# Performance work log

Measured on AMD Instinct MI355X. Metric: run time of the kernel, lower is better.

## Reference

```python
import jax, jax.numpy as jnp
import numpy as np

EPS = 1e-8  # torch.cosine_similarity norm clamp

def setup_inputs() -> dict:
    key = jax.random.key(0)
    k1, k2, k3, k4 = jax.random.split(key, 4)
    B, S, D, C = 64, 512, 768, 512
    V = jax.random.normal(k1, (B, S, D), dtype=jnp.float32)
    label_embeddings = jax.random.normal(k2, (C, D), dtype=jnp.float32)
    fc_w = jax.random.normal(k3, (C, D), dtype=jnp.float32) * 0.02
    fc_b = jax.random.normal(k4, (C,), dtype=jnp.float32) * 0.02
    return {"V": V, "label_embeddings": label_embeddings, "fc_w": fc_w, "fc_b": fc_b}

def reference(V, label_embeddings, fc_w, fc_b):
    # Normalized embeddings (cosine similarity = dot of unit vectors, norms clamped at EPS)
    Vn = V / jnp.maximum(jnp.linalg.norm(V, axis=-1, keepdims=True), EPS)
    Ln = label_embeddings / jnp.maximum(
        jnp.linalg.norm(label_embeddings, axis=-1, keepdims=True), EPS)
    # [B, S, C] cosine similarities, then max over classes -> per-token weight m [B, S]
    sims = jnp.einsum('bsd,cd->bsc', Vn, Ln)
    m = jnp.max(sims, axis=-1)
    # Softmax over sequence dim -> attention beta [B, S]
    beta = jax.nn.softmax(m, axis=-1)
    # Weighted sum of token embeddings: z = V^T beta  -> [B, D]
    z = jnp.einsum('bsd,bs->bd', V, beta)
    # Final classifier
    out = z @ fc_w.T + fc_b
    return (out, z)
```

## Files before the change

kernel.cpp:

```cpp
#include <hip/hip_runtime.h>
#include <cstdint>
#include <cstddef>

#define BB 64
#define SS 512
#define DD 768
#define CC 512

typedef __attribute__((ext_vector_type(8))) short short8;
typedef __attribute__((ext_vector_type(4))) float f32x4;

#define GLOBAL_AS __attribute__((address_space(1)))
#define LDS_AS __attribute__((address_space(3)))

static __device__ __forceinline__ unsigned short f2bf(float f) {
  union { float f; unsigned u; } v; v.f = f;
  unsigned u = v.u;
  u += 0x7FFFu + ((u >> 16) & 1u);
  return (unsigned short)(u >> 16);
}

static __device__ __forceinline__ void async_copy16(const void* g, void* l) {
  __builtin_amdgcn_global_load_lds((const GLOBAL_AS void*)g, (LDS_AS void*)l,
                                   16, 0, 0);
}

__global__ __launch_bounds__(256) void k_label_norm(const float* __restrict__ L,
                                                    unsigned short* __restrict__ Lnb) {
  const int c = blockIdx.x;
  const int tid = threadIdx.x;
  const float* row = L + (size_t)c * DD;
  float v[3];
  float s = 0.f;
#pragma unroll
  for (int k = 0; k < 3; k++) { v[k] = row[tid + 256 * k]; s += v[k] * v[k]; }
#pragma unroll
  for (int o = 32; o > 0; o >>= 1) s += __shfl_xor(s, o, 64);
  __shared__ float wsum[4];
  if ((tid & 63) == 0) wsum[tid >> 6] = s;
  __syncthreads();
  const float tot = wsum[0] + wsum[1] + wsum[2] + wsum[3];
  const float inv = 1.f / fmaxf(sqrtf(tot), 1e-8f);
  unsigned short* orow = Lnb + (size_t)c * DD;
  const int sw = c & 7;
#pragma unroll
  for (int k = 0; k < 3; k++) {
    const int d = tid + 256 * k;
    const int idx = (((d >> 3) ^ sw) << 3) | (d & 7);
    orow[idx] = f2bf(v[k] * inv);
  }
}

__global__ __launch_bounds__(512) void k_sims_max(const float* __restrict__ V,
                                                  const unsigned short* __restrict__ Lnb,
                                                  float* __restrict__ m_out) {
  const int tid = threadIdx.x;
  const int wave = tid >> 6;
  const int lane = tid & 63;
  const int q = lane >> 4;
  const int mr = lane & 15;
  const int64_t tokBase = (int64_t)blockIdx.x * 128 + wave * 16;

  __shared__ unsigned short Bs[2][16 * DD];
  __shared__ float nrmS[8][16];

  {
    const char* src = (const char*)Lnb;
    char* dst = (char*)&Bs[0][0];
#pragma unroll
    for (int i = wave; i < 24; i += 8)
      async_copy16(src + i * 1024 + lane * 16, dst + i * 1024);
  }

  const float* arow = V + (tokBase + mr) * DD + q * 8;
  short8 afrag[24];
  float nrm2 = 0.f;
#pragma unroll
  for (int kc = 0; kc < 24; kc++) {
    const float4* p = (const float4*)(arow + kc * 32);
    const float4 x = p[0];
    const float4 y = p[1];
    short8 a;
    a[0] = (short)f2bf(x.x); a[1] = (short)f2bf(x.y);
    a[2] = (short)f2bf(x.z); a[3] = (short)f2bf(x.w);
    a[4] = (short)f2bf(y.x); a[5] = (short)f2bf(y.y);
    a[6] = (short)f2bf(y.z); a[7] = (short)f2bf(y.w);
    afrag[kc] = a;
    nrm2 += x.x * x.x + x.y * x.y + x.z * x.z + x.w * x.w;
    nrm2 += y.x * y.x + y.y * y.y + y.z * y.z + y.w * y.w;
  }
  nrm2 += __shfl_xor(nrm2, 16, 64);
  nrm2 += __shfl_xor(nrm2, 32, 64);
  if (q == 0) nrmS[wave][mr] = nrm2;

  __syncthreads();

  const int swLo = mr & 3;
  const int swHi = (mr >> 2) & 1;
  const int elemBase = mr * DD + ((q ^ swLo) << 3);
  const int u0off = swHi ? 32 : 0;
  const int u1off = swHi ? 0 : 32;

  f32x4 vmax = {-3e38f, -3e38f, -3e38f, -3e38f};
  for (int cc = 0; cc < 32; cc++) {
    const int p = cc & 1;
    if (cc + 1 < 32) {
      const char* src = (const char*)(Lnb + (size_t)(cc + 1) * 16 * DD);
      char* dst = (char*)&Bs[p ^ 1][0];
#pragma unroll
      for (int i = wave; i < 24; i += 8)
        async_copy16(src + i * 1024 + lane * 16, dst + i * 1024);
    }
    const unsigned short* b0 = &Bs[p][elemBase + u0off];
    const unsigned short* b1 = &Bs[p][elemBase + u1off];
    f32x4 acc = {0.f, 0.f, 0.f, 0.f};
#pragma unroll
    for (int t = 0; t < 12; t++) {
      const short8 bu0 = *(const short8*)(b0 + t * 64);
      acc = __builtin_amdgcn_mfma_f32_16x16x32_bf16(afrag[2 * t], bu0, acc, 0, 0, 0);
      const short8 bu1 = *(const short8*)(b1 + t * 64);
      acc = __builtin_amdgcn_mfma_f32_16x16x32_bf16(afrag[2 * t + 1], bu1, acc, 0, 0, 0);
    }
    vmax[0] = fmaxf(vmax[0], acc[0]);
    vmax[1] = fmaxf(vmax[1], acc[1]);
    vmax[2] = fmaxf(vmax[2], acc[2]);
    vmax[3] = fmaxf(vmax[3], acc[3]);
    __syncthreads();
  }
#pragma unroll
  for (int o = 1; o < 16; o <<= 1) {
#pragma unroll
    for (int r = 0; r < 4; r++) vmax[r] = fmaxf(vmax[r], __shfl_xor(vmax[r], o, 64));
  }
  if (mr == 0) {
#pragma unroll
    for (int r = 0; r < 4; r++) {
      const float nr = nrmS[wave][q * 4 + r];
      m_out[tokBase + q * 4 + r] = vmax[r] / fmaxf(sqrtf(nr), 1e-8f);
    }
  }
}

__global__ __launch_bounds__(256) void k_softmax(const float* __restrict__ m,
                                                 float* __restrict__ beta) {
  const int b = blockIdx.x;
  const int tid = threadIdx.x;
  const float* mb = m + (size_t)b * SS;
  const float v0 = mb[tid];
  const float v1 = mb[tid + 256];
  float mx = fmaxf(v0, v1);
#pragma unroll
  for (int o = 32; o > 0; o >>= 1) mx = fmaxf(mx, __shfl_xor(mx, o, 64));
  __shared__ float wred[4];
  if ((tid & 63) == 0) wred[tid >> 6] = mx;
  __syncthreads();
  mx = fmaxf(fmaxf(wred[0], wred[1]), fmaxf(wred[2], wred[3]));
  const float e0 = __expf(v0 - mx);
  const float e1 = __expf(v1 - mx);
  float s = e0 + e1;
#pragma unroll
  for (int o = 32; o > 0; o >>= 1) s += __shfl_xor(s, o, 64);
  __syncthreads();
  if ((tid & 63) == 0) wred[tid >> 6] = s;
  __syncthreads();
  s = wred[0] + wred[1] + wred[2] + wred[3];
  const float inv = 1.f / s;
  float* bb = beta + (size_t)b * SS;
  bb[tid] = e0 * inv;
  bb[tid + 256] = e1 * inv;
}

__global__ __launch_bounds__(192) void k_zpart(const float* __restrict__ V,
                                               const float* __restrict__ beta,
                                               float* __restrict__ zpart,
                                               int spc, int nsc) {
  const int blk = blockIdx.x;
  const int b = blk / nsc;
  const int sc = blk % nsc;
  const int tid = threadIdx.x;
  const float* vb = V + ((size_t)b * SS + (size_t)sc * spc) * DD + tid * 4;
  const float* bb = beta + (size_t)b * SS + (size_t)sc * spc;
  float4 acc = {0.f, 0.f, 0.f, 0.f};
#pragma unroll 4
  for (int s = 0; s < spc; s++) {
    const float w = bb[s];
    const float4 x = *(const float4*)(vb + (size_t)s * DD);
    acc.x += w * x.x; acc.y += w * x.y; acc.z += w * x.z; acc.w += w * x.w;
  }
  *(float4*)(zpart + (size_t)blk * DD + tid * 4) = acc;
}

__global__ __launch_bounds__(256) void k_final(const float* __restrict__ zpart,
                                               const float* __restrict__ fc_w,
                                               const float* __restrict__ fc_b,
                                               float* __restrict__ out,
                                               float* __restrict__ zout,
                                               int nsc) {
  const int b = blockIdx.x >> 1;
  const int half = blockIdx.x & 1;
  const int tid = threadIdx.x;
  __shared__ float zs[DD];
  for (int i = tid; i < DD; i += 256) {
    float s = 0.f;
    for (int sc = 0; sc < nsc; sc++) s += zpart[((size_t)b * nsc + sc) * DD + i];
    zs[i] = s;
    if (half == 0) zout[(size_t)b * DD + i] = s;
  }
  __syncthreads();
  const int c = half * 256 + tid;
  const float4* w = (const float4*)(fc_w + (size_t)c * DD);
  float acc = 0.f;
  for (int d4 = 0; d4 < DD / 4; d4++) {
    const float4 ww = w[d4];
    acc += ww.x * zs[d4 * 4] + ww.y * zs[d4 * 4 + 1] +
           ww.z * zs[d4 * 4 + 2] + ww.w * zs[d4 * 4 + 3];
  }
  out[(size_t)b * CC + c] = acc + fc_b[c];
}

extern "C" void kernel_launch(void* const* d_in, const int* in_sizes, int n_in,
                              void* d_out, int out_size, void* d_ws, size_t ws_size,
                              hipStream_t stream) {
  const float* V  = (const float*)d_in[0];
  const float* L  = (const float*)d_in[1];
  const float* fw = (const float*)d_in[2];
  const float* fb = (const float*)d_in[3];
  float* out = (float*)d_out;

  char* ws = (char*)d_ws;
  unsigned short* Lnb = (unsigned short*)ws;
  float* m     = (float*)(ws + 786432);
  float* beta  = (float*)(ws + 917504);
  float* zpart = (float*)(ws + 1048576);

  const int nsc = (ws_size >= (size_t)1048576 + 16 * BB * DD * 4) ? 16 : 8;
  const int spc = SS / nsc;

  k_label_norm<<<CC, 256, 0, stream>>>(L, Lnb);
  k_sims_max<<<256, 512, 0, stream>>>(V, Lnb, m);
  k_softmax<<<BB, 256, 0, stream>>>(m, beta);
  k_zpart<<<BB * nsc, 192, 0, stream>>>(V, beta, zpart, spc, nsc);
  k_final<<<2 * BB, 256, 0, stream>>>(zpart, fw, fb, out, out + BB * CC, nsc);
}
```

Measured before the change: 247.4 us.

## Compute two 16-token tiles per wave in sims kernel, shrink blocks to 2 waves

Each wave in the cosine-sim max kernel now holds A fragments for 32 tokens (two 16-row tiles) and reuses each LDS-loaded label fragment for two MFMAs. Blocks shrink from 8 waves to 2 waves (64 tokens) and the grid doubles to 512 blocks. The aim is to cut LDS reads per MFMA and raise the number of independent accumulation chains. In exchange, register pressure roughly doubles (48 short8 fragments per lane), and each block now streams the whole label matrix for only 64 tokens. That doubles L2 traffic for Lnb and may lower occupancy.

```diff
diff --git a/kernel.cpp b/kernel.cpp
--- a/kernel.cpp
+++ b/kernel.cpp
@@ -51,7 +51,7 @@
   }
 }
 
-__global__ __launch_bounds__(512) void k_sims_max(const float* __restrict__ V,
+__global__ __launch_bounds__(128) void k_sims_max(const float* __restrict__ V,
                                                   const unsigned short* __restrict__ Lnb,
                                                   float* __restrict__ m_out) {
   const int tid = threadIdx.x;
@@ -59,39 +59,42 @@
   const int lane = tid & 63;
   const int q = lane >> 4;
   const int mr = lane & 15;
-  const int64_t tokBase = (int64_t)blockIdx.x * 128 + wave * 16;
+  const int64_t tokBase = (int64_t)blockIdx.x * 64 + wave * 32;
 
   __shared__ unsigned short Bs[2][16 * DD];
-  __shared__ float nrmS[8][16];
+  __shared__ float nrmS[2][2][16];
 
   {
     const char* src = (const char*)Lnb;
     char* dst = (char*)&Bs[0][0];
 #pragma unroll
-    for (int i = wave; i < 24; i += 8)
+    for (int i = wave; i < 24; i += 2)
       async_copy16(src + i * 1024 + lane * 16, dst + i * 1024);
   }
 
-  const float* arow = V + (tokBase + mr) * DD + q * 8;
-  short8 afrag[24];
-  float nrm2 = 0.f;
-#pragma unroll
-  for (int kc = 0; kc < 24; kc++) {
-    const float4* p = (const float4*)(arow + kc * 32);
-    const float4 x = p[0];
-    const float4 y = p[1];
-    short8 a;
-    a[0] = (short)f2bf(x.x); a[1] = (short)f2bf(x.y);
-    a[2] = (short)f2bf(x.z); a[3] = (short)f2bf(x.w);
-    a[4] = (short)f2bf(y.x); a[5] = (short)f2bf(y.y);
-    a[6] = (short)f2bf(y.z); a[7] = (short)f2bf(y.w);
-    afrag[kc] = a;
-    nrm2 += x.x * x.x + x.y * x.y + x.z * x.z + x.w * x.w;
-    nrm2 += y.x * y.x + y.y * y.y + y.z * y.z + y.w * y.w;
-  }
-  nrm2 += __shfl_xor(nrm2, 16, 64);
-  nrm2 += __shfl_xor(nrm2, 32, 64);
-  if (q == 0) nrmS[wave][mr] = nrm2;
+  short8 afrag[2][24];
+#pragma unroll
+  for (int s = 0; s < 2; s++) {
+    const float* arow = V + (tokBase + s * 16 + mr) * DD + q * 8;
+    float nrm2 = 0.f;
+#pragma unroll
+    for (int kc = 0; kc < 24; kc++) {
+      const float4* p = (const float4*)(arow + kc * 32);
+      const float4 x = p[0];
+      const float4 y = p[1];
+      short8 a;
+      a[0] = (short)f2bf(x.x); a[1] = (short)f2bf(x.y);
+      a[2] = (short)f2bf(x.z); a[3] = (short)f2bf(x.w);
+      a[4] = (short)f2bf(y.x); a[5] = (short)f2bf(y.y);
+      a[6] = (short)f2bf(y.z); a[7] = (short)f2bf(y.w);
+      afrag[s][kc] = a;
+      nrm2 += x.x * x.x + x.y * x.y + x.z * x.z + x.w * x.w;
+      nrm2 += y.x * y.x + y.y * y.y + y.z * y.z + y.w * y.w;
+    }
+    nrm2 += __shfl_xor(nrm2, 16, 64);
+    nrm2 += __shfl_xor(nrm2, 32, 64);
+    if (q == 0) nrmS[wave][s][mr] = nrm2;
+  }
 
   __syncthreads();
 
@@ -101,42 +104,51 @@
   const int u0off = swHi ? 32 : 0;
   const int u1off = swHi ? 0 : 32;
 
-  f32x4 vmax = {-3e38f, -3e38f, -3e38f, -3e38f};
+  f32x4 vmax0 = {-3e38f, -3e38f, -3e38f, -3e38f};
+  f32x4 vmax1 = {-3e38f, -3e38f, -3e38f, -3e38f};
   for (int cc = 0; cc < 32; cc++) {
     const int p = cc & 1;
     if (cc + 1 < 32) {
       const char* src = (const char*)(Lnb + (size_t)(cc + 1) * 16 * DD);
       char* dst = (char*)&Bs[p ^ 1][0];
 #pragma unroll
-      for (int i = wave; i < 24; i += 8)
+      for (int i = wave; i < 24; i += 2)
         async_copy16(src + i * 1024 + lane * 16, dst + i * 1024);
     }
     const unsigned short* b0 = &Bs[p][elemBase + u0off];
     const unsigned short* b1 = &Bs[p][elemBase + u1off];
-    f32x4 acc = {0.f, 0.f, 0.f, 0.f};
+    f32x4 a0 = {0.f, 0.f, 0.f, 0.f};
+    f32x4 a1 = {0.f, 0.f, 0.f, 0.f};
 #pragma unroll
     for (int t = 0; t < 12; t++) {
       const short8 bu0 = *(const short8*)(b0 + t * 64);
-      acc = __builtin_amdgcn_mfma_f32_16x16x32_bf16(afrag[2 * t], bu0, acc, 0, 0, 0);
+      a0 = __builtin_amdgcn_mfma_f32_16x16x32_bf16(afrag[0][2 * t], bu0, a0, 0, 0, 0);
+      a1 = __builtin_amdgcn_mfma_f32_16x16x32_bf16(afrag[1][2 * t], bu0, a1, 0, 0, 0);
       const short8 bu1 = *(const short8*)(b1 + t * 64);
-      acc = __builtin_amdgcn_mfma_f32_16x16x32_bf16(afrag[2 * t + 1], bu1, acc, 0, 0, 0);
-    }
-    vmax[0] = fmaxf(vmax[0], acc[0]);
-    vmax[1] = fmaxf(vmax[1], acc[1]);
-    vmax[2] = fmaxf(vmax[2], acc[2]);
-    vmax[3] = fmaxf(vmax[3], acc[3]);
+      a0 = __builtin_amdgcn_mfma_f32_16x16x32_bf16(afrag[0][2 * t + 1], bu1, a0, 0, 0, 0);
+      a1 = __builtin_amdgcn_mfma_f32_16x16x32_bf16(afrag[1][2 * t + 1], bu1, a1, 0, 0, 0);
+    }
+    vmax0[0] = fmaxf(vmax0[0], a0[0]); vmax0[1] = fmaxf(vmax0[1], a0[1]);
+    vmax0[2] = fmaxf(vmax0[2], a0[2]); vmax0[3] = fmaxf(vmax0[3], a0[3]);
+    vmax1[0] = fmaxf(vmax1[0], a1[0]); vmax1[1] = fmaxf(vmax1[1], a1[1]);
+    vmax1[2] = fmaxf(vmax1[2], a1[2]); vmax1[3] = fmaxf(vmax1[3], a1[3]);
     __syncthreads();
   }
 #pragma unroll
   for (int o = 1; o < 16; o <<= 1) {
 #pragma unroll
-    for (int r = 0; r < 4; r++) vmax[r] = fmaxf(vmax[r], __shfl_xor(vmax[r], o, 64));
+    for (int r = 0; r < 4; r++) {
+      vmax0[r] = fmaxf(vmax0[r], __shfl_xor(vmax0[r], o, 64));
+      vmax1[r] = fmaxf(vmax1[r], __shfl_xor(vmax1[r], o, 64));
+    }
   }
   if (mr == 0) {
 #pragma unroll
     for (int r = 0; r < 4; r++) {
-      const float nr = nrmS[wave][q * 4 + r];
-      m_out[tokBase + q * 4 + r] = vmax[r] / fmaxf(sqrtf(nr), 1e-8f);
+      const float n0 = nrmS[wave][0][q * 4 + r];
+      m_out[tokBase + q * 4 + r] = vmax0[r] / fmaxf(sqrtf(n0), 1e-8f);
+      const float n1 = nrmS[wave][1][q * 4 + r];
+      m_out[tokBase + 16 + q * 4 + r] = vmax1[r] / fmaxf(sqrtf(n1), 1e-8f);
     }
   }
 }
@@ -237,7 +249,7 @@
   const int spc = SS / nsc;
 
   k_label_norm<<<CC, 256, 0, stream>>>(L, Lnb);
-  k_sims_max<<<256, 512, 0, stream>>>(V, Lnb, m);
+  k_sims_max<<<512, 128, 0, stream>>>(V, Lnb, m);
   k_softmax<<<BB, 256, 0, stream>>>(m, beta);
   k_zpart<<<BB * nsc, 192, 0, stream>>>(V, beta, zpart, spc, nsc);
   k_final<<<2 * BB, 256, 0, stream>>>(zpart, fw, fb, out, out + BB * CC, nsc);
```

Result: slower. 260.2 us (+5.1%).

## Fold softmax into sims and final kernels, triple-buffer label tiles

Applied to the files above, without the earlier changes.

Removes the separate softmax kernel. The sims kernel now writes exp(m-1) directly, using the fact that cosine similarity is bounded by 1. The final kernel sums these weights per batch row and scales z by their inverse. The sims kernel is also reshaped to 256-thread blocks (twice as many blocks) with a 3-stage async LDS ring, raw s_waitcnt vmcnt and s_barrier, and one barrier per iteration. This saves a launch and one sync per iteration and overlaps loads, at the cost of relying on a fixed softmax shift and on the hand-written vmcnt counts being correct.

```diff
diff --git a/kernel.cpp b/kernel.cpp
--- a/kernel.cpp
+++ b/kernel.cpp
@@ -51,25 +51,27 @@
   }
 }
 
-__global__ __launch_bounds__(512) void k_sims_max(const float* __restrict__ V,
+__global__ __launch_bounds__(256) void k_sims_max(const float* __restrict__ V,
                                                   const unsigned short* __restrict__ Lnb,
-                                                  float* __restrict__ m_out) {
+                                                  float* __restrict__ em_out) {
   const int tid = threadIdx.x;
   const int wave = tid >> 6;
   const int lane = tid & 63;
   const int q = lane >> 4;
   const int mr = lane & 15;
-  const int64_t tokBase = (int64_t)blockIdx.x * 128 + wave * 16;
-
-  __shared__ unsigned short Bs[2][16 * DD];
-  __shared__ float nrmS[8][16];
+  const int64_t tokBase = (int64_t)blockIdx.x * 64 + wave * 16;
+
+  __shared__ unsigned short Bs[3][16 * DD];
+  __shared__ float nrmS[4][16];
 
   {
     const char* src = (const char*)Lnb;
     char* dst = (char*)&Bs[0][0];
 #pragma unroll
-    for (int i = wave; i < 24; i += 8)
+    for (int j = 0; j < 6; j++) {
+      const int i = wave + 4 * j;
       async_copy16(src + i * 1024 + lane * 16, dst + i * 1024);
+    }
   }
 
   const float* arow = V + (tokBase + mr) * DD + q * 8;
@@ -93,7 +95,15 @@
   nrm2 += __shfl_xor(nrm2, 32, 64);
   if (q == 0) nrmS[wave][mr] = nrm2;
 
-  __syncthreads();
+  {
+    const char* src = (const char*)(Lnb + (size_t)16 * DD);
+    char* dst = (char*)&Bs[1][0];
+#pragma unroll
+    for (int j = 0; j < 6; j++) {
+      const int i = wave + 4 * j;
+      async_copy16(src + i * 1024 + lane * 16, dst + i * 1024);
+    }
+  }
 
   const int swLo = mr & 3;
   const int swHi = (mr >> 2) & 1;
@@ -103,16 +113,23 @@
 
   f32x4 vmax = {-3e38f, -3e38f, -3e38f, -3e38f};
   for (int cc = 0; cc < 32; cc++) {
-    const int p = cc & 1;
-    if (cc + 1 < 32) {
-      const char* src = (const char*)(Lnb + (size_t)(cc + 1) * 16 * DD);
-      char* dst = (char*)&Bs[p ^ 1][0];
-#pragma unroll
-      for (int i = wave; i < 24; i += 8)
+    if (cc != 31) {
+      asm volatile("s_waitcnt vmcnt(6)" ::: "memory");
+    } else {
+      asm volatile("s_waitcnt vmcnt(0)" ::: "memory");
+    }
+    asm volatile("s_barrier" ::: "memory");
+    if (cc + 2 < 32) {
+      const char* src = (const char*)(Lnb + (size_t)(cc + 2) * 16 * DD);
+      char* dst = (char*)&Bs[(cc + 2) % 3][0];
+#pragma unroll
+      for (int j = 0; j < 6; j++) {
+        const int i = wave + 4 * j;
         async_copy16(src + i * 1024 + lane * 16, dst + i * 1024);
-    }
-    const unsigned short* b0 = &Bs[p][elemBase + u0off];
-    const unsigned short* b1 = &Bs[p][elemBase + u1off];
+      }
+    }
+    const unsigned short* b0 = &Bs[cc % 3][elemBase + u0off];
+    const unsigned short* b1 = &Bs[cc % 3][elemBase + u1off];
     f32x4 acc = {0.f, 0.f, 0.f, 0.f};
 #pragma unroll
     for (int t = 0; t < 12; t++) {
@@ -125,7 +142,6 @@
     vmax[1] = fmaxf(vmax[1], acc[1]);
     vmax[2] = fmaxf(vmax[2], acc[2]);
     vmax[3] = fmaxf(vmax[3], acc[3]);
-    __syncthreads();
   }
 #pragma unroll
   for (int o = 1; o < 16; o <<= 1) {
@@ -136,42 +152,14 @@
 #pragma unroll
     for (int r = 0; r < 4; r++) {
       const float nr = nrmS[wave][q * 4 + r];
-      m_out[tokBase + q * 4 + r] = vmax[r] / fmaxf(sqrtf(nr), 1e-8f);
-    }
-  }
-}
-
-__global__ __launch_bounds__(256) void k_softmax(const float* __restrict__ m,
-                                                 float* __restrict__ beta) {
-  const int b = blockIdx.x;
-  const int tid = threadIdx.x;
-  const float* mb = m + (size_t)b * SS;
-  const float v0 = mb[tid];
-  const float v1 = mb[tid + 256];
-  float mx = fmaxf(v0, v1);
-#pragma unroll
-  for (int o = 32; o > 0; o >>= 1) mx = fmaxf(mx, __shfl_xor(mx, o, 64));
-  __shared__ float wred[4];
-  if ((tid & 63) == 0) wred[tid >> 6] = mx;
-  __syncthreads();
-  mx = fmaxf(fmaxf(wred[0], wred[1]), fmaxf(wred[2], wred[3]));
-  const float e0 = __expf(v0 - mx);
-  const float e1 = __expf(v1 - mx);
-  float s = e0 + e1;
-#pragma unroll
-  for (int o = 32; o > 0; o >>= 1) s += __shfl_xor(s, o, 64);
-  __syncthreads();
-  if ((tid & 63) == 0) wred[tid >> 6] = s;
-  __syncthreads();
-  s = wred[0] + wred[1] + wred[2] + wred[3];
-  const float inv = 1.f / s;
-  float* bb = beta + (size_t)b * SS;
-  bb[tid] = e0 * inv;
-  bb[tid + 256] = e1 * inv;
+      const float m = vmax[r] / fmaxf(sqrtf(nr), 1e-8f);
+      em_out[tokBase + q * 4 + r] = __expf(m - 1.f);
+    }
+  }
 }
 
 __global__ __launch_bounds__(192) void k_zpart(const float* __restrict__ V,
-                                               const float* __restrict__ beta,
+                                               const float* __restrict__ em,
                                                float* __restrict__ zpart,
                                                int spc, int nsc) {
   const int blk = blockIdx.x;
@@ -179,7 +167,7 @@
   const int sc = blk % nsc;
   const int tid = threadIdx.x;
   const float* vb = V + ((size_t)b * SS + (size_t)sc * spc) * DD + tid * 4;
-  const float* bb = beta + (size_t)b * SS + (size_t)sc * spc;
+  const float* bb = em + (size_t)b * SS + (size_t)sc * spc;
   float4 acc = {0.f, 0.f, 0.f, 0.f};
 #pragma unroll 4
   for (int s = 0; s < spc; s++) {
@@ -191,6 +179,7 @@
 }
 
 __global__ __launch_bounds__(256) void k_final(const float* __restrict__ zpart,
+                                               const float* __restrict__ em,
                                                const float* __restrict__ fc_w,
                                                const float* __restrict__ fc_b,
                                                float* __restrict__ out,
@@ -199,10 +188,19 @@
   const int b = blockIdx.x >> 1;
   const int half = blockIdx.x & 1;
   const int tid = threadIdx.x;
+  const float* eb = em + (size_t)b * SS;
+  float es = eb[tid] + eb[tid + 256];
+#pragma unroll
+  for (int o = 32; o > 0; o >>= 1) es += __shfl_xor(es, o, 64);
+  __shared__ float wred[4];
+  if ((tid & 63) == 0) wred[tid >> 6] = es;
   __shared__ float zs[DD];
+  __syncthreads();
+  const float inv = 1.f / (wred[0] + wred[1] + wred[2] + wred[3]);
   for (int i = tid; i < DD; i += 256) {
     float s = 0.f;
     for (int sc = 0; sc < nsc; sc++) s += zpart[((size_t)b * nsc + sc) * DD + i];
+    s *= inv;
     zs[i] = s;
     if (half == 0) zout[(size_t)b * DD + i] = s;
   }
@@ -229,16 +227,14 @@
 
   char* ws = (char*)d_ws;
   unsigned short* Lnb = (unsigned short*)ws;
-  float* m     = (float*)(ws + 786432);
-  float* beta  = (float*)(ws + 917504);
+  float* em    = (float*)(ws + 786432);
   float* zpart = (float*)(ws + 1048576);
 
   const int nsc = (ws_size >= (size_t)1048576 + 16 * BB * DD * 4) ? 16 : 8;
   const int spc = SS / nsc;
 
   k_label_norm<<<CC, 256, 0, stream>>>(L, Lnb);
-  k_sims_max<<<256, 512, 0, stream>>>(V, Lnb, m);
-  k_softmax<<<BB, 256, 0, stream>>>(m, beta);
-  k_zpart<<<BB * nsc, 192, 0, stream>>>(V, beta, zpart, spc, nsc);
-  k_final<<<2 * BB, 256, 0, stream>>>(zpart, fw, fb, out, out + BB * CC, nsc);
-}
+  k_sims_max<<<512, 256, 0, stream>>>(V, Lnb, em);
+  k_zpart<<<BB * nsc, 192, 0, stream>>>(V, em, zpart, spc, nsc);
+  k_final<<<2 * BB, 256, 0, stream>>>(zpart, em, fw, fb, out, out + BB * CC, nsc);
+}
```

Measured after the change: 266.1 us. +7.5%, slower.
